# Performance work log

Measured on AMD Instinct MI355X. Metric: run time of the kernel, lower is better.

The kernel has to match this reference:

```python
import jax, jax.numpy as jnp
import numpy as np

CLAMP_MIN = 1e-30
DIAG_SCALE = 10.0


def _fast_cdist(x1, x2):
    # mean-center both by x1's row-mean (as in torch source)
    adjustment = x1.mean(axis=-2, keepdims=True)
    x1 = x1 - adjustment
    x2 = x2 - adjustment
    x1_norm = jnp.sum(x1 * x1, axis=-1, keepdims=True)  # [N,1]
    x2_norm = jnp.sum(x2 * x2, axis=-1, keepdims=True)  # [N,1]
    # matmul trick: ||a-b||^2 = ||a||^2 + ||b||^2 - 2 a.b
    res = (-2.0) * (x1 @ x2.T) + x1_norm + x2_norm.T
    return jnp.sqrt(jnp.maximum(res, CLAMP_MIN))


def reference(x):
    # L2-normalize rows
    norm = jnp.linalg.norm(x, axis=-1, keepdims=True)
    x_norm = x / norm
    dist_mat = _fast_cdist(x_norm, x_norm)  # [N, N]
    d = jnp.diagonal(dist_mat)
    dist_mat = dist_mat + DIAG_SCALE * jnp.diag(1.0 - d)
    loss = jnp.max(1.0 / dist_mat, axis=1)
    return jnp.mean(loss)


def setup_inputs() -> dict:
    key = jax.random.key(0)
    x = jax.random.normal(key, (8192, 256), dtype=jnp.float32)
    return {"x": x}
```

## Files before the change

kernel.cpp:

```cpp
#include <hip/hip_runtime.h>
#include <hip/hip_fp8.h>
#include <stdint.h>

#define N_ROWS 8192
#define N_DIM  256
#define NB     64
#define NTRI   2080

typedef __attribute__((ext_vector_type(8))) short bf16x8;
typedef __attribute__((ext_vector_type(4))) float f32x4;

__device__ inline unsigned short f2bf(float f) {
    unsigned u = __float_as_uint(f);
    unsigned r = (u + 0x7FFFu + ((u >> 16) & 1u)) >> 16;
    return (unsigned short)r;
}
__device__ inline float bf2f(unsigned short b) {
    return __uint_as_float(((unsigned)b) << 16);
}
__device__ inline unsigned encf(float f) {
    unsigned u = __float_as_uint(f);
    return u ^ ((u & 0x80000000u) ? 0xFFFFFFFFu : 0x80000000u);
}
__device__ inline float decf(unsigned e) {
    unsigned u = e ^ ((e & 0x80000000u) ? 0x80000000u : 0xFFFFFFFFu);
    return __uint_as_float(u);
}
#define ENC_BIG 0xF149F2CAu

#define GLD_LDS16(g, l)                                                        \
    __builtin_amdgcn_global_load_lds(                                          \
        (const __attribute__((address_space(1))) unsigned int*)(g),            \
        (__attribute__((address_space(3))) unsigned int*)(l), 16, 0, 0)


__global__ __launch_bounds__(256) void k_norm_fast(const float* __restrict__ x,
                                                   char* __restrict__ zf,
                                                   float* __restrict__ nsq,
                                                   unsigned* __restrict__ rmin,
                                                   float* __restrict__ out) {
    if (blockIdx.x == 0 && threadIdx.x == 0) *out = 0.0f;
    const int lane = threadIdx.x & 63;
    const int w    = threadIdx.x >> 6;
    const int row  = blockIdx.x * 4 + w;
    const float4* xr = (const float4*)(x + (size_t)row * N_DIM);
    float4 v = xr[lane];
    float ss = v.x*v.x + v.y*v.y + v.z*v.z + v.w*v.w;
    #pragma unroll
    for (int m = 1; m < 64; m <<= 1) ss += __shfl_xor(ss, m, 64);
    const float inv = 1.0f / sqrtf(ss);
    __hip_fp8_e4m3 q0(v.x * inv), q1(v.y * inv), q2(v.z * inv), q3(v.w * inv);
    unsigned packed = (unsigned)q0.__x | ((unsigned)q1.__x << 8) |
                      ((unsigned)q2.__x << 16) | ((unsigned)q3.__x << 24);
    const int k0 = lane * 4;
    *(unsigned*)(zf + ((size_t)(row >> 4) << 12) + ((k0 >> 5) << 9) +
                 (((k0 >> 3) & 3) << 7) + ((row & 15) << 3) + (k0 & 7)) = packed;
    float z0 = (float)q0, z1 = (float)q1, z2 = (float)q2, z3 = (float)q3;
    float s2 = z0*z0 + z1*z1 + z2*z2 + z3*z3;
    #pragma unroll
    for (int m = 1; m < 64; m <<= 1) s2 += __shfl_xor(s2, m, 64);
    if (lane == 0) {
        nsq[row]  = s2;
        rmin[row] = ENC_BIG;
    }
}

__global__ __launch_bounds__(256, 4) void k_gemm_fast(const char* __restrict__ zf,
                                                      const float* __restrict__ nsq,
                                                      unsigned* __restrict__ rmin) {
    __shared__ char  As[32 * 1024];
    __shared__ float pminR[128][2];
    __shared__ float pminC[128][2];

    const int tid   = threadIdx.x;
    const int lane  = tid & 63;
    const int w     = tid >> 6;
    const int waveM = (w >> 1) * 64;
    const int waveN = (w & 1) * 64;

    const int t = blockIdx.x;
    int br = (int)((129.0f - sqrtf(16641.0f - 8.0f * (float)t)) * 0.5f);
    while ((br + 1) * (129 - (br + 1)) / 2 <= t) ++br;
    while (br * (129 - br) / 2 > t) --br;
    const int bc = br + (t - br * (129 - br) / 2);
    const bool isdiag = (br == bc);

    const char* gA    = zf + (size_t)br * 32768;
    const char* laneB = zf + ((size_t)(bc * 8 + (waveN >> 4))) * 4096 + lane * 8;

    f32x4 acc[4][4];
    #pragma unroll
    for (int m = 0; m < 4; ++m)
        #pragma unroll
        for (int n = 0; n < 4; ++n)
            acc[m][n] = (f32x4){0.f, 0.f, 0.f, 0.f};

    #pragma unroll
    for (int c = 0; c < 8; ++c)
        GLD_LDS16(gA + (size_t)c * 4096 + w * 1024 + lane * 16,
                  As + c * 4096 + w * 1024);

    long bbuf[3][4];
    #pragma unroll
    for (int n = 0; n < 4; ++n) bbuf[0][n] = *(const long*)(laneB + (size_t)n * 4096 + 0 * 512);
    #pragma unroll
    for (int n = 0; n < 4; ++n) bbuf[1][n] = *(const long*)(laneB + (size_t)n * 4096 + 1 * 512);

    __syncthreads();

    #pragma unroll
    for (int g = 0; g < 8; ++g) {
        if (g + 2 < 8) {
            #pragma unroll
            for (int n = 0; n < 4; ++n)
                bbuf[(g + 2) % 3][n] =
                    *(const long*)(laneB + (size_t)n * 4096 + (g + 2) * 512);
        }
        long af[4];
        #pragma unroll
        for (int m = 0; m < 4; ++m)
            af[m] = *(const long*)&As[((waveM >> 4) + m) * 4096 + g * 512 + lane * 8];
        #pragma unroll
        for (int m = 0; m < 4; ++m)
            #pragma unroll
            for (int n = 0; n < 4; ++n)
                acc[m][n] = __builtin_amdgcn_mfma_f32_16x16x32_fp8_fp8(
                    af[m], bbuf[g % 3][n], acc[m][n], 0, 0, 0);
    }

    asm volatile("" ::: "memory");

    float nj[4];
    #pragma unroll
    for (int n = 0; n < 4; ++n)
        nj[n] = nsq[bc * 128 + waveN + n * 16 + (lane & 15)];
    float4 ni4[4];
    #pragma unroll
    for (int m = 0; m < 4; ++m)
        ni4[m] = *(const float4*)&nsq[br * 128 + waveM + m * 16 + (lane >> 4) * 4];

    float rminv[4][4];
    float cminv[4];
    #pragma unroll
    for (int m = 0; m < 4; ++m)
        #pragma unroll
        for (int r = 0; r < 4; ++r)
            rminv[m][r] = 1e30f;
    #pragma unroll
    for (int n = 0; n < 4; ++n)
        cminv[n] = 1e30f;

    const int lrow0 = waveM + (lane >> 4) * 4;
    const int lcol0 = waveN + (lane & 15);
    #pragma unroll
    for (int m = 0; m < 4; ++m) {
        #pragma unroll
        for (int r = 0; r < 4; ++r) {
            const int lr = lrow0 + m * 16 + r;
            const float nir = ((const float*)&ni4[m])[r];
            #pragma unroll
            for (int n = 0; n < 4; ++n) {
                float u = fmaf(-2.0f, acc[m][n][r], nir + nj[n]);
                const bool diag = isdiag && (lr == (lcol0 + n * 16));
                u = diag ? 1e30f : u;
                rminv[m][r] = fminf(rminv[m][r], u);
                cminv[n]    = fminf(cminv[n], u);
            }
        }
    }
    #pragma unroll
    for (int mask = 1; mask < 16; mask <<= 1)
        #pragma unroll
        for (int m = 0; m < 4; ++m)
            #pragma unroll
            for (int r = 0; r < 4; ++r)
                rminv[m][r] = fminf(rminv[m][r], __shfl_xor(rminv[m][r], mask, 64));
    if ((lane & 15) == 0) {
        const int q = lane >> 4;
        #pragma unroll
        for (int m = 0; m < 4; ++m)
            #pragma unroll
            for (int r = 0; r < 4; ++r)
                pminR[waveM + m * 16 + q * 4 + r][w & 1] = rminv[m][r];
    }
    if (!isdiag) {
        #pragma unroll
        for (int mask = 16; mask < 64; mask <<= 1)
            #pragma unroll
            for (int n = 0; n < 4; ++n)
                cminv[n] = fminf(cminv[n], __shfl_xor(cminv[n], mask, 64));
        if (lane < 16) {
            #pragma unroll
            for (int n = 0; n < 4; ++n)
                pminC[waveN + n * 16 + lane][w >> 1] = cminv[n];
        }
    }
    __syncthreads();
    if (tid < 128) {
        const float v = fminf(pminR[tid][0], pminR[tid][1]);
        atomicMin(&rmin[br * 128 + tid], encf(v));
        if (!isdiag) {
            const float vc = fminf(pminC[tid][0], pminC[tid][1]);
            atomicMin(&rmin[bc * 128 + tid], encf(vc));
        }
    }
}

__global__ __launch_bounds__(256) void k_norm_fb(const float* x,
                                                 char* zb, long zstride,
                                                 char* nsqb, long nstride,
                                                 char* rminb, long rstride,
                                                 float* out) {
    if (blockIdx.x == 0 && threadIdx.x == 0) *out = 0.0f;
    const int lane = threadIdx.x & 63;
    const int w    = threadIdx.x >> 6;
    const int row  = blockIdx.x * 4 + w;
    const float4* xr = (const float4*)(x + (size_t)row * N_DIM);
    float4 v = xr[lane];
    float ss = v.x*v.x + v.y*v.y + v.z*v.z + v.w*v.w;
    #pragma unroll
    for (int m = 1; m < 64; m <<= 1) ss += __shfl_xor(ss, m, 64);
    const float inv = 1.0f / sqrtf(ss);
    unsigned short b0 = f2bf(v.x * inv), b1 = f2bf(v.y * inv);
    unsigned short b2 = f2bf(v.z * inv), b3 = f2bf(v.w * inv);
    ushort4 uv; uv.x = b0; uv.y = b1; uv.z = b2; uv.w = b3;
    *(ushort4*)(zb + (size_t)row * zstride + lane * 8) = uv;
    float z0 = bf2f(b0), z1 = bf2f(b1), z2 = bf2f(b2), z3 = bf2f(b3);
    float s2 = z0*z0 + z1*z1 + z2*z2 + z3*z3;
    #pragma unroll
    for (int m = 1; m < 64; m <<= 1) s2 += __shfl_xor(s2, m, 64);
    if (lane == 0) {
        *(float*)(nsqb + (size_t)row * nstride) = s2;
        *(unsigned*)(rminb + (size_t)row * rstride) = ENC_BIG;
    }
}

__global__ __launch_bounds__(256, 4) void k_gemm_fb(const char* zb, long zstride,
                                                    const char* nsqb, long nstride,
                                                    char* rminb, long rstride) {
    __shared__ unsigned short As[128 * 64];
    __shared__ unsigned short Bs[128 * 64];
    __shared__ float pminR[128][2];
    __shared__ float pminC[128][2];

    const int tid   = threadIdx.x;
    const int lane  = tid & 63;
    const int w     = tid >> 6;
    const int waveM = (w >> 1) * 64;
    const int waveN = (w & 1) * 64;

    const int t = blockIdx.x;
    int br = (int)((129.0f - sqrtf(16641.0f - 8.0f * (float)t)) * 0.5f);
    while ((br + 1) * (129 - (br + 1)) / 2 <= t) ++br;
    while (br * (129 - br) / 2 > t) --br;
    const int bc = br + (t - br * (129 - br) / 2);
    const bool isdiag = (br == bc);

    const char* gA = zb + (size_t)br * 128 * zstride;
    const char* gB = zb + (size_t)bc * 128 * zstride;

    f32x4 acc[4][4];
    #pragma unroll
    for (int m = 0; m < 4; ++m)
        #pragma unroll
        for (int n = 0; n < 4; ++n)
            acc[m][n] = (f32x4){0.f, 0.f, 0.f, 0.f};

    for (int kk = 0; kk < 4; ++kk) {
        __syncthreads();
        #pragma unroll
        for (int c = 0; c < 4; ++c) {
            const int f    = c * 4096 + tid * 16;
            const int row  = f >> 7;
            const int slot = (f >> 4) & 7;
            const int c_g  = slot ^ (row & 7);
            GLD_LDS16(gA + (size_t)row * zstride + kk * 128 + c_g * 16,
                      (char*)As + c * 4096 + w * 1024);
            GLD_LDS16(gB + (size_t)row * zstride + kk * 128 + c_g * 16,
                      (char*)Bs + c * 4096 + w * 1024);
        }
        __syncthreads();

        #pragma unroll
        for (int s = 0; s < 2; ++s) {
            bf16x8 af[4], bfr[4];
            const int q = (lane >> 4) + s * 4;
            #pragma unroll
            for (int m = 0; m < 4; ++m) {
                const int rr = waveM + m * 16 + (lane & 15);
                af[m] = *(const bf16x8*)&As[rr * 64 + ((q ^ (rr & 7)) << 3)];
            }
            #pragma unroll
            for (int n = 0; n < 4; ++n) {
                const int rr = waveN + n * 16 + (lane & 15);
                bfr[n] = *(const bf16x8*)&Bs[rr * 64 + ((q ^ (rr & 7)) << 3)];
            }
            #pragma unroll
            for (int m = 0; m < 4; ++m)
                #pragma unroll
                for (int n = 0; n < 4; ++n)
                    acc[m][n] = __builtin_amdgcn_mfma_f32_16x16x32_bf16(af[m], bfr[n], acc[m][n], 0, 0, 0);
        }
    }

    asm volatile("" ::: "memory");

    float nj[4];
    #pragma unroll
    for (int n = 0; n < 4; ++n)
        nj[n] = *(const float*)(nsqb + (size_t)(bc * 128 + waveN + n * 16 + (lane & 15)) * nstride);
    float4 ni4[4];
    #pragma unroll
    for (int m = 0; m < 4; ++m) {
        const int row0 = br * 128 + waveM + m * 16 + (lane >> 4) * 4;
        ni4[m].x = *(const float*)(nsqb + (size_t)(row0 + 0) * nstride);
        ni4[m].y = *(const float*)(nsqb + (size_t)(row0 + 1) * nstride);
        ni4[m].z = *(const float*)(nsqb + (size_t)(row0 + 2) * nstride);
        ni4[m].w = *(const float*)(nsqb + (size_t)(row0 + 3) * nstride);
    }

    float rminv[4][4];
    float cminv[4];
    #pragma unroll
    for (int m = 0; m < 4; ++m)
        #pragma unroll
        for (int r = 0; r < 4; ++r)
            rminv[m][r] = 1e30f;
    #pragma unroll
    for (int n = 0; n < 4; ++n)
        cminv[n] = 1e30f;

    const int lrow0 = waveM + (lane >> 4) * 4;
    const int lcol0 = waveN + (lane & 15);
    #pragma unroll
    for (int m = 0; m < 4; ++m) {
        #pragma unroll
        for (int r = 0; r < 4; ++r) {
            const int lr = lrow0 + m * 16 + r;
            const float nir = ((const float*)&ni4[m])[r];
            #pragma unroll
            for (int n = 0; n < 4; ++n) {
                float u = fmaf(-2.0f, acc[m][n][r], nir + nj[n]);
                const bool diag = isdiag && (lr == (lcol0 + n * 16));
                u = diag ? 1e30f : u;
                rminv[m][r] = fminf(rminv[m][r], u);
                cminv[n]    = fminf(cminv[n], u);
            }
        }
    }
    #pragma unroll
    for (int mask = 1; mask < 16; mask <<= 1)
        #pragma unroll
        for (int m = 0; m < 4; ++m)
            #pragma unroll
            for (int r = 0; r < 4; ++r)
                rminv[m][r] = fminf(rminv[m][r], __shfl_xor(rminv[m][r], mask, 64));
    if ((lane & 15) == 0) {
        const int q = lane >> 4;
        #pragma unroll
        for (int m = 0; m < 4; ++m)
            #pragma unroll
            for (int r = 0; r < 4; ++r)
                pminR[waveM + m * 16 + q * 4 + r][w & 1] = rminv[m][r];
    }
    if (!isdiag) {
        #pragma unroll
        for (int mask = 16; mask < 64; mask <<= 1)
            #pragma unroll
            for (int n = 0; n < 4; ++n)
                cminv[n] = fminf(cminv[n], __shfl_xor(cminv[n], mask, 64));
        if (lane < 16) {
            #pragma unroll
            for (int n = 0; n < 4; ++n)
                pminC[waveN + n * 16 + lane][w >> 1] = cminv[n];
        }
    }
    __syncthreads();
    if (tid < 128) {
        const float v = fminf(pminR[tid][0], pminR[tid][1]);
        atomicMin((unsigned*)(rminb + (size_t)(br * 128 + tid) * rstride), encf(v));
        if (!isdiag) {
            const float vc = fminf(pminC[tid][0], pminC[tid][1]);
            atomicMin((unsigned*)(rminb + (size_t)(bc * 128 + tid) * rstride), encf(vc));
        }
    }
}

__global__ __launch_bounds__(256) void k_final(const char* nsqb, long nstride,
                                               const char* rminb, long rstride,
                                               float* out) {
    const int r = blockIdx.x * 256 + threadIdx.x;
    const float mn  = decf(*(const unsigned*)(rminb + (size_t)r * rstride));
    const float res = fmaxf(mn, 1e-30f);
    float loss = fmaxf(1.0f / sqrtf(res), 0.1f);
    #pragma unroll
    for (int m = 1; m < 64; m <<= 1) loss += __shfl_xor(loss, m, 64);
    __shared__ float wsum[4];
    const int lane = threadIdx.x & 63, w = threadIdx.x >> 6;
    if (lane == 0) wsum[w] = loss;
    __syncthreads();
    if (threadIdx.x == 0)
        atomicAdd(out, (wsum[0] + wsum[1] + wsum[2] + wsum[3]) * (1.0f / 8192.0f));
}

extern "C" void kernel_launch(void* const* d_in, const int* in_sizes, int n_in,
                              void* d_out, int out_size, void* d_ws, size_t ws_size,
                              hipStream_t stream) {
    float* x   = (float*)d_in[0];
    float* out = (float*)d_out;
    char*  ws  = (char*)d_ws;

    const size_t WS_NEED = 2u * 1024 * 1024 + 64 * 1024 + 4096;
    if (ws_size >= WS_NEED) {
        char*     zf   = ws;
        float*    nsq  = (float*)(ws + 2u * 1024 * 1024);
        unsigned* rmin = (unsigned*)(ws + 2u * 1024 * 1024 + 32 * 1024);
        k_norm_fast<<<N_ROWS / 4, 256, 0, stream>>>(x, zf, nsq, rmin, out);
        k_gemm_fast<<<NTRI, 256, 0, stream>>>(zf, nsq, rmin);
        k_final<<<N_ROWS / 256, 256, 0, stream>>>((const char*)nsq, 4,
                                                  (const char*)rmin, 4, out);
    } else {
        char* zb    = (char*)x;       long zstride = 1024;
        char* nsqb  = (char*)x + 512; long nstride = 1024;
        char* rminb = (char*)x + 516; long rstride = 1024;
        k_norm_fb<<<N_ROWS / 4, 256, 0, stream>>>(x, zb, zstride, nsqb, nstride, rminb, rstride, out);
        k_gemm_fb<<<NTRI, 256, 0, stream>>>(zb, zstride, nsqb, nstride, rminb, rstride);
        k_final<<<N_ROWS / 256, 256, 0, stream>>>(nsqb, nstride, rminb, rstride, out);
    }
}
```

Measured before the change: 81.36 us.

## Process four column tiles per block to reuse the staged A tile

```diff
diff --git a/kernel.cpp b/kernel.cpp
--- a/kernel.cpp
+++ b/kernel.cpp
@@ -6,6 +6,7 @@
 #define N_DIM  256
 #define NB     64
 #define NTRI   2080
+#define NGRP   544
 
 typedef __attribute__((ext_vector_type(8))) short bf16x8;
 typedef __attribute__((ext_vector_type(4))) float f32x4;
@@ -65,12 +66,10 @@
     }
 }
 
-__global__ __launch_bounds__(256, 4) void k_gemm_fast(const char* __restrict__ zf,
+__global__ __launch_bounds__(256, 3) void k_gemm_fast(const char* __restrict__ zf,
                                                       const float* __restrict__ nsq,
                                                       unsigned* __restrict__ rmin) {
-    __shared__ char  As[32 * 1024];
-    __shared__ float pminR[128][2];
-    __shared__ float pminC[128][2];
+    __shared__ char As[32 * 1024];
 
     const int tid   = threadIdx.x;
     const int lane  = tid & 63;
@@ -78,96 +77,119 @@
     const int waveM = (w >> 1) * 64;
     const int waveN = (w & 1) * 64;
 
-    const int t = blockIdx.x;
-    int br = (int)((129.0f - sqrtf(16641.0f - 8.0f * (float)t)) * 0.5f);
-    while ((br + 1) * (129 - (br + 1)) / 2 <= t) ++br;
-    while (br * (129 - br) / 2 > t) --br;
-    const int bc = br + (t - br * (129 - br) / 2);
-    const bool isdiag = (br == bc);
-
-    const char* gA    = zf + (size_t)br * 32768;
-    const char* laneB = zf + ((size_t)(bc * 8 + (waveN >> 4))) * 4096 + lane * 8;
-
-    f32x4 acc[4][4];
-    #pragma unroll
-    for (int m = 0; m < 4; ++m)
-        #pragma unroll
-        for (int n = 0; n < 4; ++n)
-            acc[m][n] = (f32x4){0.f, 0.f, 0.f, 0.f};
-
+    int t = blockIdx.x, br = 0;
+    while (t >= ((67 - br) >> 2)) { t -= (67 - br) >> 2; ++br; }
+    const int bc0 = br + t * 4;
+    const int nc  = (64 - bc0 < 4) ? (64 - bc0) : 4;
+    int bcs[4];
+    #pragma unroll
+    for (int ci = 0; ci < 4; ++ci)
+        bcs[ci] = (bc0 + ci < 63) ? bc0 + ci : 63;
+
+    const char* gA = zf + (size_t)br * 32768;
     #pragma unroll
     for (int c = 0; c < 8; ++c)
         GLD_LDS16(gA + (size_t)c * 4096 + w * 1024 + lane * 16,
                   As + c * 4096 + w * 1024);
 
-    long bbuf[3][4];
-    #pragma unroll
-    for (int n = 0; n < 4; ++n) bbuf[0][n] = *(const long*)(laneB + (size_t)n * 4096 + 0 * 512);
-    #pragma unroll
-    for (int n = 0; n < 4; ++n) bbuf[1][n] = *(const long*)(laneB + (size_t)n * 4096 + 1 * 512);
-
-    __syncthreads();
-
-    #pragma unroll
-    for (int g = 0; g < 8; ++g) {
-        if (g + 2 < 8) {
-            #pragma unroll
-            for (int n = 0; n < 4; ++n)
-                bbuf[(g + 2) % 3][n] =
-                    *(const long*)(laneB + (size_t)n * 4096 + (g + 2) * 512);
-        }
-        long af[4];
-        #pragma unroll
-        for (int m = 0; m < 4; ++m)
-            af[m] = *(const long*)&As[((waveM >> 4) + m) * 4096 + g * 512 + lane * 8];
-        #pragma unroll
-        for (int m = 0; m < 4; ++m)
-            #pragma unroll
-            for (int n = 0; n < 4; ++n)
-                acc[m][n] = __builtin_amdgcn_mfma_f32_16x16x32_fp8_fp8(
-                    af[m], bbuf[g % 3][n], acc[m][n], 0, 0, 0);
-    }
-
-    asm volatile("" ::: "memory");
-
-    float nj[4];
-    #pragma unroll
-    for (int n = 0; n < 4; ++n)
-        nj[n] = nsq[bc * 128 + waveN + n * 16 + (lane & 15)];
+    float njall[4][4];
+    #pragma unroll
+    for (int ci = 0; ci < 4; ++ci)
+        #pragma unroll
+        for (int n = 0; n < 4; ++n)
+            njall[ci][n] = nsq[bcs[ci] * 128 + waveN + n * 16 + (lane & 15)];
     float4 ni4[4];
     #pragma unroll
     for (int m = 0; m < 4; ++m)
         ni4[m] = *(const float4*)&nsq[br * 128 + waveM + m * 16 + (lane >> 4) * 4];
 
+    const char* laneB0 = zf + ((size_t)(waveN >> 4)) * 4096 + lane * 8;
+#define BADDR(s) (laneB0 + ((size_t)bcs[(s) >> 3] * 32768) + (size_t)nn * 4096 + ((s) & 7) * 512)
+    long bbuf[4][4];
+    #pragma unroll
+    for (int s = 0; s < 3; ++s)
+        #pragma unroll
+        for (int nn = 0; nn < 4; ++nn)
+            bbuf[s][nn] = *(const long*)BADDR(s);
+
     float rminv[4][4];
-    float cminv[4];
     #pragma unroll
     for (int m = 0; m < 4; ++m)
         #pragma unroll
         for (int r = 0; r < 4; ++r)
             rminv[m][r] = 1e30f;
-    #pragma unroll
-    for (int n = 0; n < 4; ++n)
-        cminv[n] = 1e30f;
 
     const int lrow0 = waveM + (lane >> 4) * 4;
     const int lcol0 = waveN + (lane & 15);
-    #pragma unroll
-    for (int m = 0; m < 4; ++m) {
-        #pragma unroll
-        for (int r = 0; r < 4; ++r) {
-            const int lr = lrow0 + m * 16 + r;
-            const float nir = ((const float*)&ni4[m])[r];
-            #pragma unroll
-            for (int n = 0; n < 4; ++n) {
-                float u = fmaf(-2.0f, acc[m][n][r], nir + nj[n]);
-                const bool diag = isdiag && (lr == (lcol0 + n * 16));
-                u = diag ? 1e30f : u;
-                rminv[m][r] = fminf(rminv[m][r], u);
-                cminv[n]    = fminf(cminv[n], u);
-            }
-        }
-    }
+
+    __syncthreads();
+
+    #pragma unroll
+    for (int ci = 0; ci < 4; ++ci) {
+        const bool act    = ci < nc;
+        const bool cidiag = act && (bcs[ci] == br);
+        f32x4 acc[4][4];
+        #pragma unroll
+        for (int m = 0; m < 4; ++m)
+            #pragma unroll
+            for (int n = 0; n < 4; ++n)
+                acc[m][n] = (f32x4){0.f, 0.f, 0.f, 0.f};
+
+        #pragma unroll
+        for (int g = 0; g < 8; ++g) {
+            const int s = ci * 8 + g;
+            if (s + 3 < 32) {
+                #pragma unroll
+                for (int nn = 0; nn < 4; ++nn)
+                    bbuf[(s + 3) & 3][nn] = *(const long*)BADDR(s + 3);
+            }
+            long af[4];
+            #pragma unroll
+            for (int m = 0; m < 4; ++m)
+                af[m] = *(const long*)&As[((waveM >> 4) + m) * 4096 + g * 512 + lane * 8];
+            #pragma unroll
+            for (int m = 0; m < 4; ++m)
+                #pragma unroll
+                for (int n = 0; n < 4; ++n)
+                    acc[m][n] = __builtin_amdgcn_mfma_f32_16x16x32_fp8_fp8(
+                        af[m], bbuf[s & 3][n], acc[m][n], 0, 0, 0);
+        }
+
+        float cminv[4];
+        #pragma unroll
+        for (int n = 0; n < 4; ++n)
+            cminv[n] = 1e30f;
+        #pragma unroll
+        for (int m = 0; m < 4; ++m) {
+            #pragma unroll
+            for (int r = 0; r < 4; ++r) {
+                const int lr  = lrow0 + m * 16 + r;
+                const float nir = ((const float*)&ni4[m])[r];
+                #pragma unroll
+                for (int n = 0; n < 4; ++n) {
+                    float u = fmaf(-2.0f, acc[m][n][r], nir + njall[ci][n]);
+                    const bool kill = !act || (cidiag && (lr == (lcol0 + n * 16)));
+                    u = kill ? 1e30f : u;
+                    rminv[m][r] = fminf(rminv[m][r], u);
+                    cminv[n]    = fminf(cminv[n], u);
+                }
+            }
+        }
+        if (!cidiag) {
+            #pragma unroll
+            for (int mask = 16; mask < 64; mask <<= 1)
+                #pragma unroll
+                for (int n = 0; n < 4; ++n)
+                    cminv[n] = fminf(cminv[n], __shfl_xor(cminv[n], mask, 64));
+            if (act && lane < 16) {
+                #pragma unroll
+                for (int n = 0; n < 4; ++n)
+                    atomicMin(&rmin[bcs[ci] * 128 + waveN + n * 16 + lane], encf(cminv[n]));
+            }
+        }
+    }
+#undef BADDR
+
     #pragma unroll
     for (int mask = 1; mask < 16; mask <<= 1)
         #pragma unroll
@@ -181,28 +203,8 @@
         for (int m = 0; m < 4; ++m)
             #pragma unroll
             for (int r = 0; r < 4; ++r)
-                pminR[waveM + m * 16 + q * 4 + r][w & 1] = rminv[m][r];
-    }
-    if (!isdiag) {
-        #pragma unroll
-        for (int mask = 16; mask < 64; mask <<= 1)
-            #pragma unroll
-            for (int n = 0; n < 4; ++n)
-                cminv[n] = fminf(cminv[n], __shfl_xor(cminv[n], mask, 64));
-        if (lane < 16) {
-            #pragma unroll
-            for (int n = 0; n < 4; ++n)
-                pminC[waveN + n * 16 + lane][w >> 1] = cminv[n];
-        }
-    }
-    __syncthreads();
-    if (tid < 128) {
-        const float v = fminf(pminR[tid][0], pminR[tid][1]);
-        atomicMin(&rmin[br * 128 + tid], encf(v));
-        if (!isdiag) {
-            const float vc = fminf(pminC[tid][0], pminC[tid][1]);
-            atomicMin(&rmin[bc * 128 + tid], encf(vc));
-        }
+                atomicMin(&rmin[br * 128 + waveM + m * 16 + q * 4 + r],
+                          encf(rminv[m][r]));
     }
 }
 
@@ -416,7 +418,7 @@
         float*    nsq  = (float*)(ws + 2u * 1024 * 1024);
         unsigned* rmin = (unsigned*)(ws + 2u * 1024 * 1024 + 32 * 1024);
         k_norm_fast<<<N_ROWS / 4, 256, 0, stream>>>(x, zf, nsq, rmin, out);
-        k_gemm_fast<<<NTRI, 256, 0, stream>>>(zf, nsq, rmin);
+        k_gemm_fast<<<NGRP, 256, 0, stream>>>(zf, nsq, rmin);
         k_final<<<N_ROWS / 256, 256, 0, stream>>>((const char*)nsq, 4,
                                                   (const char*)rmin, 4, out);
     } else {
```

Result: slower. 136.8 us (+68.1%).
